# Optimization experiments

Measured on AMD Instinct MI355X. Metric: run time of the kernel, lower is better.

Reference implementation:

```python
import jax, jax.numpy as jnp
import numpy as np

B, C, D, H, W = 2, 32, 16, 64, 64
SCALER = 8
CK = C // SCALER  # qk channels = 4


def setup_inputs() -> dict:
    key = jax.random.key(0)
    ks = jax.random.split(key, 8)
    s = 0.05
    return {
        "x": jax.random.normal(ks[0], (B, C, D, H, W), dtype=jnp.float32),
        "Wk": jax.random.normal(ks[1], (CK, C), dtype=jnp.float32) * s,
        "bk": jax.random.normal(ks[2], (CK,), dtype=jnp.float32) * s,
        "Wq": jax.random.normal(ks[3], (CK, C), dtype=jnp.float32) * s,
        "bq": jax.random.normal(ks[4], (CK,), dtype=jnp.float32) * s,
        "Wv": jax.random.normal(ks[5], (C, C), dtype=jnp.float32) * s,
        "bv": jax.random.normal(ks[6], (C,), dtype=jnp.float32) * s,
        "gamma": jnp.ones((1,), dtype=jnp.float32),
    }


def _proj(x, Wt, b):
    # 1x1x1 Conv3d == channel matmul: (o,c) x (b,c,d,h,w) -> (b,o,d,h,w)
    y = jnp.einsum('oc,bcdhw->bodhw', Wt, x) + b[None, :, None, None, None]
    return y


def reference(x, Wk, bk, Wq, bq, Wv, bv, gamma):
    b, c, d, h, w = x.shape
    hw = h * w
    xk = _proj(x, Wk, bk).reshape(b, -1, hw)   # (b, ck*d, hw)
    xq = _proj(x, Wq, bq).reshape(b, -1, hw)   # (b, ck*d, hw)
    xv = _proj(x, Wv, bv).reshape(b, -1, hw)   # (b, c*d,  hw)
    # dot[b,i,j] = sum_e xk[b,e,i] * xq[b,e,j]  -> (b, hw, hw)
    dot = jnp.einsum('bei,bej->bij', xk, xq)
    att = jax.nn.softmax(dot, axis=-1)          # softmax over last dim
    # x_a[b,m,i] = sum_j xv[b,m,j] * att[b,i,j]
    x_a = jnp.einsum('bmj,bij->bmi', xv, att)
    x_a = x_a.reshape(b, c, d, h, w)
    return gamma[0] * x + x_a
```

## Files before the change

kernel.cpp:

```cpp
#include <hip/hip_runtime.h>
#include <hip/hip_bf16.h>

#define B_   2
#define C_   32
#define D_   16
#define HW_  4096
#define CK_  4
#define E_   64
#define M_   512
#define JC_  4

typedef __attribute__((ext_vector_type(8)))  short bf16x8;
typedef __attribute__((ext_vector_type(16))) float f32x16;
typedef __attribute__((ext_vector_type(2)))  unsigned int u32x2;

union U4 { unsigned int u[4]; bf16x8 v; };

__device__ __forceinline__ short f2bf(float f) {
    __hip_bfloat16 h = __float2bfloat16(f);
    return *reinterpret_cast<short*>(&h);
}
__device__ __forceinline__ unsigned short f2bfu(float f) {
    __hip_bfloat16 h = __float2bfloat16(f);
    return *reinterpret_cast<unsigned short*>(&h);
}

__global__ __launch_bounds__(256) void proj_kernel(
    const float* __restrict__ x,
    const float* __restrict__ Wk, const float* __restrict__ bk,
    const float* __restrict__ Wq, const float* __restrict__ bq,
    const float* __restrict__ Wv, const float* __restrict__ bv,
    short* __restrict__ xk, short* __restrict__ xq,
    __hip_bfloat16* __restrict__ v)
{
    __shared__ short s_k[32*16], s_q[32*16];
    const int t    = threadIdx.x;
    const int lane = t & 63;
    const int w    = t >> 6;
    const int h    = lane >> 5;
    const int c    = lane & 31;

    const int pt = blockIdx.x & 127;
    const int dg = (blockIdx.x >> 7) & 3;
    const int b  = blockIdx.x >> 9;
    const int d  = dg*4 + w;
    const int p0 = pt*32;

    bf16x8 af[2][2];
    #pragma unroll
    for (int s = 0; s < 2; ++s) {
        const float* wv = Wv + c*C_ + s*16 + h*8;
        #pragma unroll
        for (int k = 0; k < 8; ++k) af[0][s][k] = f2bf(wv[k]);
        const float* wu = (c < 4) ? (Wk + c*C_ + s*16 + h*8)
                        : (c < 8) ? (Wq + (c-4)*C_ + s*16 + h*8) : nullptr;
        #pragma unroll
        for (int k = 0; k < 8; ++k) af[1][s][k] = f2bf(wu ? wu[k] : 0.f);
    }

    U4 xb[2];
    #pragma unroll
    for (int s = 0; s < 2; ++s) {
        #pragma unroll
        for (int j = 0; j < 4; ++j) {
            int c0 = s*16 + h*8 + 2*j;
            union { float f; unsigned int u; } ua, ub;
            ua.f = x[(((size_t)(b*C_ + c0  )*D_ + d)*HW_) + p0 + c];
            ub.f = x[(((size_t)(b*C_ + c0+1)*D_ + d)*HW_) + p0 + c];
            xb[s].u[j] = __builtin_amdgcn_perm(ub.u, ua.u, 0x07060302);
        }
    }

    f32x16 a0, a1;
    #pragma unroll
    for (int r = 0; r < 16; ++r) { a0[r] = 0.f; a1[r] = 0.f; }
    #pragma unroll
    for (int s = 0; s < 2; ++s) {
        a0 = __builtin_amdgcn_mfma_f32_32x32x16_bf16(af[0][s], xb[s].v, a0, 0, 0, 0);
        a1 = __builtin_amdgcn_mfma_f32_32x32x16_bf16(af[1][s], xb[s].v, a1, 0, 0, 0);
    }

    #pragma unroll
    for (int r = 0; r < 16; ++r) {
        int o = (r & 3) + 8*(r >> 2) + 4*h;
        v[((size_t)b*M_ + (o*D_ + d))*HW_ + p0 + c] = __float2bfloat16(a0[r] + bv[o]);
    }

    #pragma unroll
    for (int r = 0; r < 4; ++r) {
        if (h == 0) s_k[c*16 + w*4 + r] = f2bf(a1[r] + bk[r]);
        else        s_q[c*16 + w*4 + r] = f2bf(a1[r] + bq[r]);
    }
    __syncthreads();

    const int p = t >> 3, seg = t & 7;
    size_t gb = ((size_t)b*HW_ + p0 + p)*E_ + dg*16 + seg*2;
    *(unsigned int*)(xk + gb) = *(const unsigned int*)(&s_k[p*16 + seg*2]);
    *(unsigned int*)(xq + gb) = *(const unsigned int*)(&s_q[p*16 + seg*2]);
}

__device__ __forceinline__ void load_lds16(const short* g, short* l) {
    __builtin_amdgcn_global_load_lds((const __attribute__((address_space(1))) void*)g,
                                     (__attribute__((address_space(3))) void*)l,
                                     16, 0, 0);
}

__global__ __launch_bounds__(256, 4) void attn_kernel(
    const short* __restrict__ xk_, const short* __restrict__ xq_,
    const short* __restrict__ v_,
    unsigned short* __restrict__ Op, float* __restrict__ lw)
{
    __shared__ short s_xq[2][2048];
    __shared__ short s_v [2][4096];

    const int t    = threadIdx.x;
    const int lane = t & 63;
    const int w    = t >> 6;
    const int h    = lane >> 5;
    const int c    = lane & 31;

    const int cls  = blockIdx.x & 7;
    const int b    = cls >> 2, mg = cls & 3;
    const int rest = blockIdx.x >> 3;
    const int ig   = rest & 31;
    const int jc   = rest >> 5;
    const int i0   = ig*128 + w*32;
    const int jbase = jc*(HW_/JC_);

    const short* xk_g = xk_ + (size_t)b*HW_*E_;
    const short* xq_g = xq_ + (size_t)b*HW_*E_;
    const short* v_g  = v_  + (size_t)b*M_*HW_ + (size_t)mg*128*HW_;

    bf16x8 kb[4];
    #pragma unroll
    for (int s = 0; s < 4; ++s)
        kb[s] = *(const bf16x8*)(xk_g + (size_t)(i0 + c)*E_ + s*16 + h*8);

    f32x16 acc[4];
    #pragma unroll
    for (int mt = 0; mt < 4; ++mt)
        #pragma unroll
        for (int r = 0; r < 16; ++r) acc[mt][r] = 0.f;
    float lp = 0.f;

    auto stage = [&](int buf, int j0) {
        {
            int r_ = w*8 + (lane>>3), cc = (lane&7) ^ (r_&7);
            load_lds16(xq_g + (size_t)(j0 + r_)*E_ + cc*8, &s_xq[buf][w*512]);
        }
        #pragma unroll
        for (int k = 0; k < 2; ++k) {
            int r0 = w*32 + k*16;
            int r_ = r0 + (lane>>2);
            int g  = (lane&3) ^ ((r_>>1)&3);
            load_lds16(v_g + (size_t)r_*HW_ + j0 + g*8, &s_v[buf][r0*32]);
        }
    };

    stage(0, jbase);
    __syncthreads();

    for (int it = 0; it < (HW_/JC_)/32; ++it) {
        const int cur = it & 1;
        if (it + 1 < (HW_/JC_)/32)
            stage(cur^1, jbase + (it+1)*32);

        f32x16 st;
        #pragma unroll
        for (int r = 0; r < 16; ++r) st[r] = 0.f;
        __builtin_amdgcn_s_setprio(1);
        #pragma unroll
        for (int s = 0; s < 4; ++s) {
            int slot = (s*2 + h) ^ (c & 7);
            bf16x8 a1 = *(const bf16x8*)(&s_xq[cur][c*64 + slot*8]);
            st = __builtin_amdgcn_mfma_f32_32x32x16_bf16(a1, kb[s], st, 0, 0, 0);
        }
        __builtin_amdgcn_s_setprio(0);

        unsigned int dq[8];
        #pragma unroll
        for (int qd = 0; qd < 8; ++qd) {
            union { float f; unsigned int u; } ua, ub;
            float e0 = __expf(st[2*qd]);
            float e1 = __expf(st[2*qd+1]);
            lp += e0 + e1;
            ua.f = e0; ub.f = e1;
            dq[qd] = __builtin_amdgcn_perm(ub.u, ua.u, 0x07060302);
        }

        U4 a2[2];
        {
            u32x2 r02 = __builtin_amdgcn_permlane32_swap(dq[0], dq[2], false, false);
            u32x2 r13 = __builtin_amdgcn_permlane32_swap(dq[1], dq[3], false, false);
            u32x2 r46 = __builtin_amdgcn_permlane32_swap(dq[4], dq[6], false, false);
            u32x2 r57 = __builtin_amdgcn_permlane32_swap(dq[5], dq[7], false, false);
            a2[0].u[0] = r02[0]; a2[0].u[1] = r13[0];
            a2[0].u[2] = r02[1]; a2[0].u[3] = r13[1];
            a2[1].u[0] = r46[0]; a2[1].u[1] = r57[0];
            a2[1].u[2] = r46[1]; a2[1].u[3] = r57[1];
        }

        __builtin_amdgcn_s_setprio(1);
        #pragma unroll
        for (int s2 = 0; s2 < 2; ++s2) {
            #pragma unroll
            for (int mt = 0; mt < 4; ++mt) {
                int rowm = mt*32 + c;
                int slot = (s2*2 + h) ^ ((rowm>>1)&3);
                bf16x8 vb = *(const bf16x8*)(&s_v[cur][rowm*32 + slot*8]);
                acc[mt] = __builtin_amdgcn_mfma_f32_32x32x16_bf16(a2[s2].v, vb, acc[mt], 0, 0, 0);
            }
        }
        __builtin_amdgcn_s_setprio(0);
        __syncthreads();
    }

    float l = lp + __shfl_xor(lp, 32, 64);
    if (h == 0 && mg == 0)
        lw[(size_t)(jc*B_ + b)*HW_ + i0 + c] = l;

    const size_t opb = ((size_t)(jc*B_ + b)*M_ + mg*128)*HW_;
    #pragma unroll
    for (int mt = 0; mt < 4; ++mt) {
        size_t rb = opb + (size_t)(mt*32 + c)*HW_ + i0;
        #pragma unroll
        for (int g = 0; g < 4; ++g) {
            ushort4 s4;
            s4.x = f2bfu(acc[mt][4*g+0]);
            s4.y = f2bfu(acc[mt][4*g+1]);
            s4.z = f2bfu(acc[mt][4*g+2]);
            s4.w = f2bfu(acc[mt][4*g+3]);
            *(ushort4*)(Op + rb + 8*g + 4*h) = s4;
        }
    }
}

__global__ __launch_bounds__(256) void reduce_kernel(
    const float* __restrict__ x, const float* __restrict__ gamma_p,
    const unsigned short* __restrict__ Op, const float* __restrict__ lw,
    float* __restrict__ out)
{
    size_t idx = ((size_t)blockIdx.x*256 + threadIdx.x)*4;
    int i = idx & (HW_-1);
    size_t bm = idx >> 12;
    int m = bm & (M_-1);
    int b = (int)(bm >> 9);

    float4 o = {0.f,0.f,0.f,0.f};
    float4 l = {0.f,0.f,0.f,0.f};
    #pragma unroll
    for (int jc = 0; jc < JC_; ++jc) {
        ushort4 ov = *(const ushort4*)(Op + ((size_t)(jc*B_ + b)*M_ + m)*HW_ + i);
        o.x += __uint_as_float((unsigned int)ov.x << 16);
        o.y += __uint_as_float((unsigned int)ov.y << 16);
        o.z += __uint_as_float((unsigned int)ov.z << 16);
        o.w += __uint_as_float((unsigned int)ov.w << 16);
        float4 lv = *(const float4*)(lw + (size_t)(jc*B_ + b)*HW_ + i);
        l.x += lv.x; l.y += lv.y; l.z += lv.z; l.w += lv.w;
    }
    const float gamma = gamma_p[0];
    float4 xv = *(const float4*)(x + idx);
    float4 r;
    r.x = gamma*xv.x + o.x / l.x;
    r.y = gamma*xv.y + o.y / l.y;
    r.z = gamma*xv.z + o.z / l.z;
    r.w = gamma*xv.w + o.w / l.w;
    *(float4*)(out + idx) = r;
}

extern "C" void kernel_launch(void* const* d_in, const int* in_sizes, int n_in,
                              void* d_out, int out_size, void* d_ws, size_t ws_size,
                              hipStream_t stream)
{
    const float* x     = (const float*)d_in[0];
    const float* Wk    = (const float*)d_in[1];
    const float* bk    = (const float*)d_in[2];
    const float* Wq    = (const float*)d_in[3];
    const float* bq    = (const float*)d_in[4];
    const float* Wv    = (const float*)d_in[5];
    const float* bv    = (const float*)d_in[6];
    const float* gamma = (const float*)d_in[7];
    float* out = (float*)d_out;

    char* ws = (char*)d_ws;
    short*          xk   = (short*)(ws);
    short*          xq   = (short*)(ws + (1<<20));
    short*          v    = (short*)(ws + (2<<20));
    unsigned short* Op   = (unsigned short*)(ws + (10<<20) + 8192);
    float*          lw   = (float*)(ws + (10<<20) + 8192
                                    + (size_t)JC_*B_*M_*HW_*2);

    proj_kernel<<<B_*(D_/4)*(HW_/32), 256, 0, stream>>>(x, Wk, bk, Wq, bq, Wv, bv,
                                                        xk, xq, (__hip_bfloat16*)v);
    attn_kernel<<<8*32*JC_, 256, 0, stream>>>(xk, xq, v, Op, lw);
    reduce_kernel<<<(B_*M_*HW_)/(256*4), 256, 0, stream>>>(x, gamma, Op, lw, out);
}
```

Baseline: 161.8 us.

## Share softmax probabilities across two M-groups via LDS in 512-thread attention blocks

The attention kernel now uses 512-thread blocks that cover 256 value channels instead of 128. The first four waves compute the QK scores and exp once, then publish the bf16 probabilities to LDS for the second four waves. This halves the redundant QK MFMA and exp work, which was previously repeated in every M-group block. In exchange it adds an extra intra-iteration barrier, an LDS round-trip for P, and an imbalanced wave schedule where only half the waves stage xq and do softmax.

```diff
diff --git a/kernel.cpp b/kernel.cpp
--- a/kernel.cpp
+++ b/kernel.cpp
@@ -105,36 +105,44 @@
                                      16, 0, 0);
 }
 
-__global__ __launch_bounds__(256, 4) void attn_kernel(
+__global__ __launch_bounds__(512, 4) void attn_kernel(
     const short* __restrict__ xk_, const short* __restrict__ xq_,
     const short* __restrict__ v_,
     unsigned short* __restrict__ Op, float* __restrict__ lw)
 {
     __shared__ short s_xq[2][2048];
-    __shared__ short s_v [2][4096];
+    __shared__ short s_v [2][8192];
+    __shared__ short s_p [4][1024];
 
     const int t    = threadIdx.x;
     const int lane = t & 63;
     const int w    = t >> 6;
+    const int wm   = w >> 2;
+    const int wi   = w & 3;
     const int h    = lane >> 5;
     const int c    = lane & 31;
+    const int q    = (lane >> 2) & 1;
 
     const int cls  = blockIdx.x & 7;
-    const int b    = cls >> 2, mg = cls & 3;
+    const int b    = cls >> 2;
+    const int mgp  = (cls >> 1) & 1;
+    const int igl  = cls & 1;
     const int rest = blockIdx.x >> 3;
-    const int ig   = rest & 31;
-    const int jc   = rest >> 5;
-    const int i0   = ig*128 + w*32;
+    const int ig   = (rest & 15)*2 + igl;
+    const int jc   = rest >> 4;
+    const int i0   = ig*128 + wi*32;
     const int jbase = jc*(HW_/JC_);
 
     const short* xk_g = xk_ + (size_t)b*HW_*E_;
     const short* xq_g = xq_ + (size_t)b*HW_*E_;
-    const short* v_g  = v_  + (size_t)b*M_*HW_ + (size_t)mg*128*HW_;
+    const short* v_g  = v_  + (size_t)b*M_*HW_ + (size_t)mgp*256*HW_;
 
     bf16x8 kb[4];
-    #pragma unroll
-    for (int s = 0; s < 4; ++s)
-        kb[s] = *(const bf16x8*)(xk_g + (size_t)(i0 + c)*E_ + s*16 + h*8);
+    if (wm == 0) {
+        #pragma unroll
+        for (int s = 0; s < 4; ++s)
+            kb[s] = *(const bf16x8*)(xk_g + (size_t)(i0 + c)*E_ + s*16 + h*8);
+    }
 
     f32x16 acc[4];
     #pragma unroll
@@ -144,16 +152,17 @@
     float lp = 0.f;
 
     auto stage = [&](int buf, int j0) {
-        {
-            int r_ = w*8 + (lane>>3), cc = (lane&7) ^ (r_&7);
-            load_lds16(xq_g + (size_t)(j0 + r_)*E_ + cc*8, &s_xq[buf][w*512]);
-        }
-        #pragma unroll
-        for (int k = 0; k < 2; ++k) {
-            int r0 = w*32 + k*16;
-            int r_ = r0 + (lane>>2);
-            int g  = (lane&3) ^ ((r_>>1)&3);
-            load_lds16(v_g + (size_t)r_*HW_ + j0 + g*8, &s_v[buf][r0*32]);
+        if (wm == 0) {
+            int r_ = wi*8 + (lane>>3), cc = (lane&7) ^ (r_&7);
+            load_lds16(xq_g + (size_t)(j0 + r_)*E_ + cc*8, &s_xq[buf][wi*512]);
+        } else {
+            #pragma unroll
+            for (int k = 0; k < 4; ++k) {
+                int r0 = wi*64 + k*16;
+                int r_ = r0 + (lane>>2);
+                int g  = (lane&3) ^ ((r_>>1)&3);
+                load_lds16(v_g + (size_t)r_*HW_ + j0 + g*8, &s_v[buf][r0*32]);
+            }
         }
     };
 
@@ -165,61 +174,98 @@
         if (it + 1 < (HW_/JC_)/32)
             stage(cur^1, jbase + (it+1)*32);
 
-        f32x16 st;
-        #pragma unroll
-        for (int r = 0; r < 16; ++r) st[r] = 0.f;
-        __builtin_amdgcn_s_setprio(1);
-        #pragma unroll
-        for (int s = 0; s < 4; ++s) {
-            int slot = (s*2 + h) ^ (c & 7);
-            bf16x8 a1 = *(const bf16x8*)(&s_xq[cur][c*64 + slot*8]);
-            st = __builtin_amdgcn_mfma_f32_32x32x16_bf16(a1, kb[s], st, 0, 0, 0);
+        bf16x8 vb0[4];
+        if (wm == 0) {
+            f32x16 st;
+            #pragma unroll
+            for (int r = 0; r < 16; ++r) st[r] = 0.f;
+            __builtin_amdgcn_s_setprio(1);
+            #pragma unroll
+            for (int s = 0; s < 4; ++s) {
+                int slot = (s*2 + h) ^ (c & 7);
+                bf16x8 a1 = *(const bf16x8*)(&s_xq[cur][c*64 + slot*8]);
+                st = __builtin_amdgcn_mfma_f32_32x32x16_bf16(a1, kb[s], st, 0, 0, 0);
+            }
+            __builtin_amdgcn_s_setprio(0);
+
+            unsigned int dq[8];
+            #pragma unroll
+            for (int qd = 0; qd < 8; ++qd) {
+                union { float f; unsigned int u; } ua, ub;
+                float e0 = __expf(st[2*qd]);
+                float e1 = __expf(st[2*qd+1]);
+                lp += e0 + e1;
+                ua.f = e0; ub.f = e1;
+                dq[qd] = __builtin_amdgcn_perm(ub.u, ua.u, 0x07060302);
+            }
+
+            U4 a2[2];
+            {
+                u32x2 r02 = __builtin_amdgcn_permlane32_swap(dq[0], dq[2], false, false);
+                u32x2 r13 = __builtin_amdgcn_permlane32_swap(dq[1], dq[3], false, false);
+                u32x2 r46 = __builtin_amdgcn_permlane32_swap(dq[4], dq[6], false, false);
+                u32x2 r57 = __builtin_amdgcn_permlane32_swap(dq[5], dq[7], false, false);
+                a2[0].u[0] = r02[0]; a2[0].u[1] = r13[0];
+                a2[0].u[2] = r02[1]; a2[0].u[3] = r13[1];
+                a2[1].u[0] = r46[0]; a2[1].u[1] = r57[0];
+                a2[1].u[2] = r46[1]; a2[1].u[3] = r57[1];
+            }
+
+            *(bf16x8*)(&s_p[wi][lane*16 + q*8])     = a2[0].v;
+            *(bf16x8*)(&s_p[wi][lane*16 + (1^q)*8]) = a2[1].v;
+            asm volatile("s_waitcnt lgkmcnt(0)" ::: "memory");
+            __builtin_amdgcn_sched_barrier(0);
+            __builtin_amdgcn_s_barrier();
+            asm volatile("" ::: "memory");
+
+            __builtin_amdgcn_s_setprio(1);
+            #pragma unroll
+            for (int s2 = 0; s2 < 2; ++s2) {
+                #pragma unroll
+                for (int mt = 0; mt < 4; ++mt) {
+                    int rowm = mt*32 + c;
+                    int slot = (s2*2 + h) ^ ((rowm>>1)&3);
+                    bf16x8 vb = *(const bf16x8*)(&s_v[cur][rowm*32 + slot*8]);
+                    acc[mt] = __builtin_amdgcn_mfma_f32_32x32x16_bf16(a2[s2].v, vb, acc[mt], 0, 0, 0);
+                }
+            }
+            __builtin_amdgcn_s_setprio(0);
+        } else {
+            #pragma unroll
+            for (int mt = 0; mt < 4; ++mt) {
+                int rowm = 128 + mt*32 + c;
+                int slot = (0*2 + h) ^ ((rowm>>1)&3);
+                vb0[mt] = *(const bf16x8*)(&s_v[cur][rowm*32 + slot*8]);
+            }
+            __builtin_amdgcn_sched_barrier(0);
+            __builtin_amdgcn_s_barrier();
+            asm volatile("" ::: "memory");
+
+            U4 a2c[2];
+            a2c[0].v = *(const bf16x8*)(&s_p[wi][lane*16 + q*8]);
+            a2c[1].v = *(const bf16x8*)(&s_p[wi][lane*16 + (1^q)*8]);
+            __builtin_amdgcn_s_setprio(1);
+            #pragma unroll
+            for (int mt = 0; mt < 4; ++mt)
+                acc[mt] = __builtin_amdgcn_mfma_f32_32x32x16_bf16(a2c[0].v, vb0[mt], acc[mt], 0, 0, 0);
+            #pragma unroll
+            for (int mt = 0; mt < 4; ++mt) {
+                int rowm = 128 + mt*32 + c;
+                int slot = (1*2 + h) ^ ((rowm>>1)&3);
+                bf16x8 vb = *(const bf16x8*)(&s_v[cur][rowm*32 + slot*8]);
+                acc[mt] = __builtin_amdgcn_mfma_f32_32x32x16_bf16(a2c[1].v, vb, acc[mt], 0, 0, 0);
+            }
+            __builtin_amdgcn_s_setprio(0);
         }
-        __builtin_amdgcn_s_setprio(0);
-
-        unsigned int dq[8];
-        #pragma unroll
-        for (int qd = 0; qd < 8; ++qd) {
-            union { float f; unsigned int u; } ua, ub;
-            float e0 = __expf(st[2*qd]);
-            float e1 = __expf(st[2*qd+1]);
-            lp += e0 + e1;
-            ua.f = e0; ub.f = e1;
-            dq[qd] = __builtin_amdgcn_perm(ub.u, ua.u, 0x07060302);
-        }
-
-        U4 a2[2];
-        {
-            u32x2 r02 = __builtin_amdgcn_permlane32_swap(dq[0], dq[2], false, false);
-            u32x2 r13 = __builtin_amdgcn_permlane32_swap(dq[1], dq[3], false, false);
-            u32x2 r46 = __builtin_amdgcn_permlane32_swap(dq[4], dq[6], false, false);
-            u32x2 r57 = __builtin_amdgcn_permlane32_swap(dq[5], dq[7], false, false);
-            a2[0].u[0] = r02[0]; a2[0].u[1] = r13[0];
-            a2[0].u[2] = r02[1]; a2[0].u[3] = r13[1];
-            a2[1].u[0] = r46[0]; a2[1].u[1] = r57[0];
-            a2[1].u[2] = r46[1]; a2[1].u[3] = r57[1];
-        }
-
-        __builtin_amdgcn_s_setprio(1);
-        #pragma unroll
-        for (int s2 = 0; s2 < 2; ++s2) {
-            #pragma unroll
-            for (int mt = 0; mt < 4; ++mt) {
-                int rowm = mt*32 + c;
-                int slot = (s2*2 + h) ^ ((rowm>>1)&3);
-                bf16x8 vb = *(const bf16x8*)(&s_v[cur][rowm*32 + slot*8]);
-                acc[mt] = __builtin_amdgcn_mfma_f32_32x32x16_bf16(a2[s2].v, vb, acc[mt], 0, 0, 0);
-            }
-        }
-        __builtin_amdgcn_s_setprio(0);
+
         __syncthreads();
     }
 
     float l = lp + __shfl_xor(lp, 32, 64);
-    if (h == 0 && mg == 0)
+    if (wm == 0 && h == 0 && mgp == 0)
         lw[(size_t)(jc*B_ + b)*HW_ + i0 + c] = l;
 
-    const size_t opb = ((size_t)(jc*B_ + b)*M_ + mg*128)*HW_;
+    const size_t opb = ((size_t)(jc*B_ + b)*M_ + mgp*256 + wm*128)*HW_;
     #pragma unroll
     for (int mt = 0; mt < 4; ++mt) {
         size_t rb = opb + (size_t)(mt*32 + c)*HW_ + i0;
@@ -292,6 +338,6 @@
 
     proj_kernel<<<B_*(D_/4)*(HW_/32), 256, 0, stream>>>(x, Wk, bk, Wq, bq, Wv, bv,
                                                         xk, xq, (__hip_bfloat16*)v);
-    attn_kernel<<<8*32*JC_, 256, 0, stream>>>(xk, xq, v, Op, lw);
+    attn_kernel<<<8*64, 512, 0, stream>>>(xk, xq, v, Op, lw);
     reduce_kernel<<<(B_*M_*HW_)/(256*4), 256, 0, stream>>>(x, gamma, Op, lw, out);
 }
```

After: 195.1 us. +20.6%, slower.
